# Optimization experiments

Hardware: AMD Instinct MI355X
Metric: run time of the kernel (lower is better)

## Reference

```python
import jax, jax.numpy as jnp
import numpy as np

EPS = 1e-5
K_UP = 5      # k_upsample
SCALE = 2

def _conv(x, w, pad):
    # NCHW conv, no bias
    return jax.lax.conv_general_dilated(
        x, w, window_strides=(1, 1), padding=((pad, pad), (pad, pad)),
        dimension_numbers=('NCHW', 'OIHW', 'NCHW'))

def _bn(x, gamma, beta):
    # train-mode BatchNorm2d forward: batch stats over (N,H,W), biased var
    m = x.mean(axis=(0, 2, 3), keepdims=True)
    v = x.var(axis=(0, 2, 3), keepdims=True)
    xn = (x - m) * jax.lax.rsqrt(v + EPS)
    return xn * gamma[None, :, None, None] + beta[None, :, None, None]

def _pixel_shuffle(x, r):
    b, c, h, w = x.shape
    co = c // (r * r)
    x = x.reshape(b, co, r, r, h, w)
    x = x.transpose(0, 1, 4, 2, 5, 3)  # b, co, h, r, w, r
    return x.reshape(b, co, h * r, w * r)

def setup_inputs() -> dict:
    key = jax.random.key(0)
    ks = jax.random.split(key, 3)
    b, c, h, w = 8, 128, 64, 64
    mid = 64
    return {
        'x': jax.random.normal(ks[0], (b, c, h, w), jnp.float32),
        'comp_w': jax.random.normal(ks[1], (mid, c, 1, 1), jnp.float32) * (1.0 / np.sqrt(c)),
        'comp_g': jnp.ones((mid,), jnp.float32),
        'comp_b': jnp.zeros((mid,), jnp.float32),
        'enc_w': jax.random.normal(ks[2], ((K_UP * SCALE) ** 2, mid, 3, 3), jnp.float32) * (1.0 / np.sqrt(mid * 9)),
        'enc_g': jnp.ones(((K_UP * SCALE) ** 2,), jnp.float32),
        'enc_b': jnp.zeros(((K_UP * SCALE) ** 2,), jnp.float32),
    }

def reference(x, comp_w, comp_g, comp_b, enc_w, enc_g, enc_b):
    b, c, h, w = x.shape
    hm, wm = h * SCALE, w * SCALE
    # --- kernel prediction branch ---
    t = jax.nn.silu(_bn(_conv(x, comp_w, 0), comp_g, comp_b))        # [b,64,h,w]
    t = _bn(_conv(t, enc_w, 1), enc_g, enc_b)                        # [b,100,h,w] (act=False)
    t = _pixel_shuffle(t, SCALE)                                     # [b,25,hm,wm]
    wgt = jax.nn.softmax(t, axis=1)                                  # [b,25,hm,wm]
    # --- feature reassembly branch ---
    x_up = jnp.repeat(jnp.repeat(x, SCALE, axis=2), SCALE, axis=3)   # nearest upsample
    pad = (K_UP // 2) * SCALE  # = 4, preserves hm x wm with dilation=SCALE
    xp = jnp.pad(x_up, ((0, 0), (0, 0), (pad, pad), (pad, pad)))
    # unfold: kernel K_UP, dilation SCALE -> [b, c, 25, hm, wm], taps in (kh, kw) order
    patches = jnp.stack(
        [xp[:, :, dy * SCALE:dy * SCALE + hm, dx * SCALE:dx * SCALE + wm]
         for dy in range(K_UP) for dx in range(K_UP)], axis=2)
    # content-aware weighted sum over the 25 taps
    return jnp.einsum('bkhw,bckhw->bchw', wgt, patches)
```

## Files before the change

kernel.cpp:

```cpp
#include <hip/hip_runtime.h>
#include <hip/hip_bf16.h>
#include <math.h>

#define C_   128
#define HW_  4096
#define OC_  100
#define NSTAT_ 32768.0f

typedef __bf16 bf16x8 __attribute__((ext_vector_type(8)));
typedef __bf16 bf16x4 __attribute__((ext_vector_type(4)));
typedef float  f32x4  __attribute__((ext_vector_type(4)));

__global__ __launch_bounds__(256, 4) void k_conv1(const float* __restrict__ x,
                                                  const float* __restrict__ w,
                                                  const float* __restrict__ wenc,
                                                  __bf16* __restrict__ t1c,
                                                  float* __restrict__ csum,
                                                  float* __restrict__ csq,
                                                  __bf16* __restrict__ wprep) {
    __shared__ __bf16 xt[64 * 128];
    __shared__ __bf16 wt[64 * 128];
    __shared__ float sS[64], sQ[64];

    int blk = blockIdx.x;
    int b = blk & 7;
    int chunk = blk >> 3;
    int px0 = chunk * 64;
    int tid = threadIdx.x;
    if (tid < 64) { sS[tid] = 0.f; sQ[tid] = 0.f; }

    if (blk < 63) {
#pragma unroll
        for (int u = 0; u < 4; ++u) {
            int idx = blk * 1024 + u * 256 + tid;
            int oc = idx / 576, k = idx - oc * 576;
            int tap = k >> 6, ic = k & 63;
            wprep[idx] = (oc < OC_) ? (__bf16)wenc[((size_t)oc * 64 + ic) * 9 + tap]
                                    : (__bf16)0.f;
        }
    }

#pragma unroll
    for (int it = 0; it < 8; ++it) {
        int j = it * 256 + tid;
        int oc = j >> 5, f = j & 31;
        float4 v = *(const float4*)(w + (size_t)oc * 128 + f * 4);
        int blki = (f >> 1) ^ (oc & 15);
        bf16x4 st;
        st[0] = (__bf16)v.x; st[1] = (__bf16)v.y; st[2] = (__bf16)v.z; st[3] = (__bf16)v.w;
        *(bf16x4*)&wt[oc * 128 + blki * 8 + (f & 1) * 4] = st;
    }
#pragma unroll
    for (int it = 0; it < 2; ++it) {
        int j = it * 256 + tid;
        int px4 = (j & 15) * 4, icq = j >> 4;
        const float* xp = x + ((size_t)b * C_ + icq * 4) * HW_ + px0 + px4;
        float4 v0 = *(const float4*)(xp);
        float4 v1 = *(const float4*)(xp + HW_);
        float4 v2 = *(const float4*)(xp + 2 * HW_);
        float4 v3 = *(const float4*)(xp + 3 * HW_);
        float r0[4] = {v0.x, v0.y, v0.z, v0.w};
        float r1[4] = {v1.x, v1.y, v1.z, v1.w};
        float r2_[4] = {v2.x, v2.y, v2.z, v2.w};
        float r3[4] = {v3.x, v3.y, v3.z, v3.w};
#pragma unroll
        for (int r2 = 0; r2 < 4; ++r2) {
            int px = px4 + r2;
            int blki = (icq >> 1) ^ (px & 15);
            bf16x4 st;
            st[0] = (__bf16)r0[r2]; st[1] = (__bf16)r1[r2];
            st[2] = (__bf16)r2_[r2]; st[3] = (__bf16)r3[r2];
            *(bf16x4*)&xt[px * 128 + blki * 8 + (icq & 1) * 4] = st;
        }
    }
    __syncthreads();

    int lane = tid & 63, wv = tid >> 6;
    int p = lane & 15, q = lane >> 4;

    f32x4 acc[4];
#pragma unroll
    for (int n = 0; n < 4; ++n) acc[n] = (f32x4){0.f, 0.f, 0.f, 0.f};

#pragma unroll
    for (int kk = 0; kk < 4; ++kk) {
        int blki = (kk * 4 + q) ^ p;
        bf16x8 a = *(const bf16x8*)&xt[(wv * 16 + p) * 128 + blki * 8];
#pragma unroll
        for (int n = 0; n < 4; ++n) {
            bf16x8 bb = *(const bf16x8*)&wt[(n * 16 + p) * 128 + blki * 8];
            acc[n] = __builtin_amdgcn_mfma_f32_16x16x32_bf16(a, bb, acc[n], 0, 0, 0);
        }
    }

    __bf16* t1b = t1c + ((size_t)b * HW_ + px0 + wv * 16) * 64;
#pragma unroll
    for (int n = 0; n < 4; ++n) {
        float s = 0.f, qq = 0.f;
#pragma unroll
        for (int rg = 0; rg < 4; ++rg) {
            float v = acc[n][rg];
            t1b[(size_t)(q * 4 + rg) * 64 + n * 16 + p] = (__bf16)v;
            s += v; qq += v * v;
        }
        s += __shfl_down(s, 32, 64);  s += __shfl_down(s, 16, 64);
        qq += __shfl_down(qq, 32, 64); qq += __shfl_down(qq, 16, 64);
        if (lane < 16) {
            atomicAdd(&sS[n * 16 + p], s);
            atomicAdd(&sQ[n * 16 + p], qq);
        }
    }
    __syncthreads();
    if (tid < 64) {
        atomicAdd(&csum[tid], sS[tid]);
        atomicAdd(&csq[tid], sQ[tid]);
    }
}

__global__ __launch_bounds__(256, 4) void k_conv3(const __bf16* __restrict__ t1c,
                                                  const __bf16* __restrict__ wprep,
                                                  const float* __restrict__ csum,
                                                  const float* __restrict__ csq,
                                                  const float* __restrict__ cg,
                                                  const float* __restrict__ cb,
                                                  float* __restrict__ t2c,
                                                  float* __restrict__ esum,
                                                  float* __restrict__ esq) {
    __shared__ __bf16 xt[10 * 10 * 72];
    __shared__ __bf16 bt[2][112 * 32];
    __shared__ float lsc[64], lsh[64];
    __shared__ float esuml[112], esql[112];

    int blk = blockIdx.x;
    int b = blk & 7;
    int tile = blk >> 3;
    int ty0 = (tile >> 3) * 8, tx0 = (tile & 7) * 8;
    int tid = threadIdx.x;
    if (tid < 112) { esuml[tid] = 0.f; esql[tid] = 0.f; }
    if (tid >= 128 && tid < 192) {
        int c = tid - 128;
        float invN = 1.0f / NSTAT_;
        float m = csum[c] * invN;
        float v = csq[c] * invN - m * m;
        float rs = rsqrtf(v + 1e-5f);
        float sc = cg[c] * rs;
        lsc[c] = sc;
        lsh[c] = cb[c] - m * sc;
    }
    __syncthreads();

    {
        int oc = tid >> 2, part = tid & 3;
        *(bf16x8*)&bt[0][oc * 32 + part * 8] =
            *(const bf16x8*)(wprep + (size_t)oc * 576 + part * 8);
        if (tid < 192) {
            int c1 = tid + 256;
            int oc1 = c1 >> 2, p1 = c1 & 3;
            *(bf16x8*)&bt[0][oc1 * 32 + p1 * 8] =
                *(const bf16x8*)(wprep + (size_t)oc1 * 576 + p1 * 8);
        }
    }

    const __bf16* tb = t1c + (size_t)b * HW_ * 64;
#pragma unroll
    for (int it = 0; it < 7; ++it) {
        int idx = it * 256 + tid;
        if (idx < 1600) {
            int pxi = idx >> 4, f4 = idx & 15;
            int yy = pxi / 10, xx = pxi - yy * 10;
            int gy = ty0 + yy - 1, gx = tx0 + xx - 1;
            float o0 = 0.f, o1 = 0.f, o2 = 0.f, o3 = 0.f;
            if (gy >= 0 && gy < 64 && gx >= 0 && gx < 64) {
                bf16x4 v = *(const bf16x4*)(tb + ((size_t)(gy << 6) + gx) * 64 + f4 * 4);
                float4 sc = *(const float4*)(lsc + f4 * 4);
                float4 sh = *(const float4*)(lsh + f4 * 4);
                float u;
                u = fmaf((float)v[0], sc.x, sh.x); o0 = u / (1.f + __expf(-u));
                u = fmaf((float)v[1], sc.y, sh.y); o1 = u / (1.f + __expf(-u));
                u = fmaf((float)v[2], sc.z, sh.z); o2 = u / (1.f + __expf(-u));
                u = fmaf((float)v[3], sc.w, sh.w); o3 = u / (1.f + __expf(-u));
            }
            bf16x4 st;
            st[0] = (__bf16)o0; st[1] = (__bf16)o1; st[2] = (__bf16)o2; st[3] = (__bf16)o3;
            *(bf16x4*)&xt[pxi * 72 + f4 * 4] = st;
        }
    }
    __syncthreads();

    int lane = tid & 63, wv = tid >> 6;
    int p = lane & 15, q = lane >> 4;
    int ya = 2 * wv + (p >> 3), xa = p & 7;
    int soc = tid >> 2, spart = tid & 3;
    int soc1 = (tid + 256) >> 2, spart1 = (tid + 256) & 3;

    f32x4 acc[7];
#pragma unroll
    for (int n = 0; n < 7; ++n) acc[n] = (f32x4){0.f, 0.f, 0.f, 0.f};

#pragma unroll
    for (int kk = 0; kk < 18; ++kk) {
        const int cur = kk & 1;
        bf16x8 r0, r1;
        if (kk < 17) {
            r0 = *(const bf16x8*)(wprep + (size_t)soc * 576 + (kk + 1) * 32 + spart * 8);
            if (tid < 192)
                r1 = *(const bf16x8*)(wprep + (size_t)soc1 * 576 + (kk + 1) * 32 + spart1 * 8);
        }
        const int tap = kk >> 1, ich = (kk & 1) * 32;
        const int ky = tap / 3, kx = tap - ky * 3;
        bf16x8 a0 = *(const bf16x8*)&xt[((ya + ky) * 10 + xa + kx) * 72 + ich + q * 8];
#pragma unroll
        for (int n = 0; n < 7; ++n) {
            bf16x8 bb = *(const bf16x8*)&bt[cur][(n * 16 + p) * 32 + q * 8];
            acc[n] = __builtin_amdgcn_mfma_f32_16x16x32_bf16(a0, bb, acc[n], 0, 0, 0);
        }
        if (kk < 17) {
            *(bf16x8*)&bt[1 - cur][soc * 32 + spart * 8] = r0;
            if (tid < 192)
                *(bf16x8*)&bt[1 - cur][soc1 * 32 + spart1 * 8] = r1;
            __syncthreads();
        }
    }

    float* t2b = t2c + (size_t)b * 25 * HW_ * 4;
#pragma unroll
    for (int n = 0; n < 7; ++n) {
        int oc = n * 16 + p;
        int k5 = oc >> 2, sch = oc & 3;
        bool wr = oc < OC_;
        float s = 0.f, qq = 0.f;
#pragma unroll
        for (int rg = 0; rg < 4; ++rg) {
            int mp = q * 4 + rg;
            int y = ty0 + 2 * wv + (mp >> 3), xo = tx0 + (mp & 7);
            float v = acc[n][rg];
            if (wr) t2b[((size_t)k5 * HW_ + (y << 6) + xo) * 4 + sch] = v;
            s += v; qq += v * v;
        }
        s += __shfl_down(s, 32, 64);  s += __shfl_down(s, 16, 64);
        qq += __shfl_down(qq, 32, 64); qq += __shfl_down(qq, 16, 64);
        if (lane < 16) {
            atomicAdd(&esuml[n * 16 + lane], s);
            atomicAdd(&esql[n * 16 + lane], qq);
        }
    }
    __syncthreads();
    if (tid < 112) {
        atomicAdd(&esum[tid], esuml[tid]);
        atomicAdd(&esq[tid], esql[tid]);
    }
}

__global__ __launch_bounds__(512, 2) void k_carafe(const float* __restrict__ x,
                                                   const float* __restrict__ t2c,
                                                   const float* __restrict__ esum,
                                                   const float* __restrict__ esq,
                                                   const float* __restrict__ eg,
                                                   const float* __restrict__ eb,
                                                   float* __restrict__ out) {
    __shared__ float xt[400 * 20];
    __shared__ float esc[112], esh[112];

    int blk = blockIdx.x;
    int b = blk & 7;
    int r = blk >> 3;
    int tile = r & 15;
    int cq = r >> 4;
    int tx0 = (tile & 3) * 16, ty0 = (tile >> 2) * 16;
    int tid = threadIdx.x;
    if (tid < 112) {
        float invN = 1.0f / NSTAT_;
        float m = esum[tid] * invN;
        float v = esq[tid] * invN - m * m;
        float rs = rsqrtf(v + 1e-5f);
        float sc = (tid < OC_) ? eg[tid] * rs : 0.f;
        esc[tid] = sc;
        esh[tid] = (tid < OC_) ? eb[tid] - m * sc : 0.f;
    }

    int t0 = tid & 1, px = tid >> 1;
    int pxx = px & 15, py = px >> 4;
    int iy = ty0 + py, jx = tx0 + pxx;
    int pxl = (iy << 6) + jx;

    const float* xb = x + (size_t)b * C_ * HW_;

    f32x4 pf[4];
#pragma unroll
    for (int it = 0; it < 4; ++it) {
        int idx = it * 512 + tid;
        if (idx < 1600) {
            int c4 = idx / 400;
            int hp = idx - c4 * 400;
            int yy = hp / 20, xx = hp - yy * 20;
            int gy = ty0 - 2 + yy, gx = tx0 - 2 + xx;
            f32x4 st = {0.f, 0.f, 0.f, 0.f};
            if (gy >= 0 && gy < 64 && gx >= 0 && gx < 64) {
                size_t base = (size_t)(cq * 32 + c4 * 4) * HW_ + (gy << 6) + gx;
                st[0] = xb[base];
                st[1] = xb[base + HW_];
                st[2] = xb[base + 2 * HW_];
                st[3] = xb[base + 3 * HW_];
            }
            pf[it] = st;
        }
    }
    __syncthreads();

    float wA[25], wB[25];
    {
        const float* t2p = t2c + (size_t)b * 25 * HW_ * 4 + (size_t)pxl * 4 + 2 * t0;
        int cA = 2 * t0, cB = 2 * t0 + 1;
        float mxA = -1e30f, mxB = -1e30f;
#pragma unroll
        for (int k = 0; k < 25; ++k) {
            float2 v = *(const float2*)(t2p + (size_t)k * HW_ * 4);
            float lA = fmaf(v.x, esc[4 * k + cA], esh[4 * k + cA]);
            float lB = fmaf(v.y, esc[4 * k + cB], esh[4 * k + cB]);
            wA[k] = lA; wB[k] = lB;
            mxA = fmaxf(mxA, lA); mxB = fmaxf(mxB, lB);
        }
        float sA = 0.f, sB = 0.f;
#pragma unroll
        for (int k = 0; k < 25; ++k) {
            float eA = __expf(wA[k] - mxA);
            float eB = __expf(wB[k] - mxB);
            wA[k] = eA; wB[k] = eB;
            sA += eA; sB += eB;
        }
        float iA = 1.f / sA, iB = 1.f / sB;
#pragma unroll
        for (int k = 0; k < 25; ++k) { wA[k] *= iA; wB[k] *= iB; }
    }

#pragma unroll
    for (int it = 0; it < 4; ++it) {
        int idx = it * 512 + tid;
        if (idx < 1600) {
            int c4 = idx / 400;
            int hp = idx - c4 * 400;
            *(f32x4*)&xt[hp * 20 + c4 * 4] = pf[it];
        }
    }
    __syncthreads();

    int i0 = iy * 2 + t0;
    float* op = out + (size_t)b * C_ * 16384 + (size_t)i0 * 128 + jx * 2;
    int cbase = cq * 32;

    f32x4 pg[4];
#pragma unroll
    for (int it = 0; it < 4; ++it) {
        int idx = it * 512 + tid;
        if (idx < 1600) {
            int c4 = idx / 400;
            int hp = idx - c4 * 400;
            int yy = hp / 20, xx = hp - yy * 20;
            int gy = ty0 - 2 + yy, gx = tx0 - 2 + xx;
            f32x4 st = {0.f, 0.f, 0.f, 0.f};
            if (gy >= 0 && gy < 64 && gx >= 0 && gx < 64) {
                size_t base = (size_t)(cbase + 16 + c4 * 4) * HW_ + (gy << 6) + gx;
                st[0] = xb[base];
                st[1] = xb[base + HW_];
                st[2] = xb[base + 2 * HW_];
                st[3] = xb[base + 3 * HW_];
            }
            pg[it] = st;
        }
    }

    {
        float accA[16], accB[16];
#pragma unroll
        for (int e = 0; e < 16; ++e) { accA[e] = 0.f; accB[e] = 0.f; }
#pragma unroll
        for (int dy = 0; dy < 5; ++dy)
#pragma unroll
            for (int dx = 0; dx < 5; ++dx) {
                int pos = (py + dy) * 20 + pxx + dx;
                float a = wA[dy * 5 + dx], bw = wB[dy * 5 + dx];
#pragma unroll
                for (int c4 = 0; c4 < 4; ++c4) {
                    f32x4 xv = *(const f32x4*)&xt[pos * 20 + c4 * 4];
                    accA[c4 * 4 + 0] = fmaf(a, xv[0], accA[c4 * 4 + 0]);
                    accA[c4 * 4 + 1] = fmaf(a, xv[1], accA[c4 * 4 + 1]);
                    accA[c4 * 4 + 2] = fmaf(a, xv[2], accA[c4 * 4 + 2]);
                    accA[c4 * 4 + 3] = fmaf(a, xv[3], accA[c4 * 4 + 3]);
                    accB[c4 * 4 + 0] = fmaf(bw, xv[0], accB[c4 * 4 + 0]);
                    accB[c4 * 4 + 1] = fmaf(bw, xv[1], accB[c4 * 4 + 1]);
                    accB[c4 * 4 + 2] = fmaf(bw, xv[2], accB[c4 * 4 + 2]);
                    accB[c4 * 4 + 3] = fmaf(bw, xv[3], accB[c4 * 4 + 3]);
                }
            }
#pragma unroll
        for (int e = 0; e < 16; ++e) {
            float2 st2;
            st2.x = accA[e]; st2.y = accB[e];
            *(float2*)&op[(size_t)(cbase + e) * 16384] = st2;
        }
    }
    __syncthreads();

#pragma unroll
    for (int it = 0; it < 4; ++it) {
        int idx = it * 512 + tid;
        if (idx < 1600) {
            int c4 = idx / 400;
            int hp = idx - c4 * 400;
            *(f32x4*)&xt[hp * 20 + c4 * 4] = pg[it];
        }
    }
    __syncthreads();

    {
        float accA[16], accB[16];
#pragma unroll
        for (int e = 0; e < 16; ++e) { accA[e] = 0.f; accB[e] = 0.f; }
#pragma unroll
        for (int dy = 0; dy < 5; ++dy)
#pragma unroll
            for (int dx = 0; dx < 5; ++dx) {
                int pos = (py + dy) * 20 + pxx + dx;
                float a = wA[dy * 5 + dx], bw = wB[dy * 5 + dx];
#pragma unroll
                for (int c4 = 0; c4 < 4; ++c4) {
                    f32x4 xv = *(const f32x4*)&xt[pos * 20 + c4 * 4];
                    accA[c4 * 4 + 0] = fmaf(a, xv[0], accA[c4 * 4 + 0]);
                    accA[c4 * 4 + 1] = fmaf(a, xv[1], accA[c4 * 4 + 1]);
                    accA[c4 * 4 + 2] = fmaf(a, xv[2], accA[c4 * 4 + 2]);
                    accA[c4 * 4 + 3] = fmaf(a, xv[3], accA[c4 * 4 + 3]);
                    accB[c4 * 4 + 0] = fmaf(bw, xv[0], accB[c4 * 4 + 0]);
                    accB[c4 * 4 + 1] = fmaf(bw, xv[1], accB[c4 * 4 + 1]);
                    accB[c4 * 4 + 2] = fmaf(bw, xv[2], accB[c4 * 4 + 2]);
                    accB[c4 * 4 + 3] = fmaf(bw, xv[3], accB[c4 * 4 + 3]);
                }
            }
#pragma unroll
        for (int e = 0; e < 16; ++e) {
            float2 st2;
            st2.x = accA[e]; st2.y = accB[e];
            *(float2*)&op[(size_t)(cbase + 16 + e) * 16384] = st2;
        }
    }
}

extern "C" void kernel_launch(void* const* d_in, const int* in_sizes, int n_in,
                              void* d_out, int out_size, void* d_ws, size_t ws_size,
                              hipStream_t stream) {
    const float* x      = (const float*)d_in[0];
    const float* comp_w = (const float*)d_in[1];
    const float* comp_g = (const float*)d_in[2];
    const float* comp_b = (const float*)d_in[3];
    const float* enc_w  = (const float*)d_in[4];
    const float* enc_g  = (const float*)d_in[5];
    const float* enc_b  = (const float*)d_in[6];
    float* out = (float*)d_out;

    float* ws = (float*)d_ws;
    __bf16* t1c = (__bf16*)ws;
    float* t2c  = ws + 1048576;
    float* st   = ws + 1048576 + 3670016;
    float* csum = st;
    float* csq  = st + 64;
    float* esum = st + 128;
    float* esq  = st + 240;
    __bf16* wprep = (__bf16*)(st + 352);

    hipMemsetAsync(st, 0, 352 * sizeof(float), stream);
    k_conv1<<<512, 256, 0, stream>>>(x, comp_w, enc_w, t1c, csum, csq, wprep);
    k_conv3<<<512, 256, 0, stream>>>(t1c, wprep, csum, csq, comp_g, comp_b, t2c, esum, esq);
    k_carafe<<<512, 512, 0, stream>>>(x, t2c, esum, esq, enc_g, enc_b, out);
}
```

Measured before the change: 158.7 us.

## Read conv3 weights directly from global and stage output tile through LDS

The k_conv3 kernel no longer double-buffers the encoder weights in shared memory with a barrier per K-step. Each lane now loads its MFMA B-fragment straight from global memory (relying on cache). The accumulator results are written into the reused input-tile LDS buffer and then stored to global as coalesced 16-byte vectors instead of scattered scalar stores. This removes 17 barriers and the LDS weight footprint, at the cost of more global/L2 weight traffic per wave.

```diff
diff --git a/kernel.cpp b/kernel.cpp
--- a/kernel.cpp
+++ b/kernel.cpp
@@ -126,8 +126,8 @@
                                                   float* __restrict__ t2c,
                                                   float* __restrict__ esum,
                                                   float* __restrict__ esq) {
-    __shared__ __bf16 xt[10 * 10 * 72];
-    __shared__ __bf16 bt[2][112 * 32];
+    __shared__ float xtf[25 * 260];
+    __bf16* xt = (__bf16*)xtf;
     __shared__ float lsc[64], lsh[64];
     __shared__ float esuml[112], esql[112];
 
@@ -148,18 +148,6 @@
         lsh[c] = cb[c] - m * sc;
     }
     __syncthreads();
-
-    {
-        int oc = tid >> 2, part = tid & 3;
-        *(bf16x8*)&bt[0][oc * 32 + part * 8] =
-            *(const bf16x8*)(wprep + (size_t)oc * 576 + part * 8);
-        if (tid < 192) {
-            int c1 = tid + 256;
-            int oc1 = c1 >> 2, p1 = c1 & 3;
-            *(bf16x8*)&bt[0][oc1 * 32 + p1 * 8] =
-                *(const bf16x8*)(wprep + (size_t)oc1 * 576 + p1 * 8);
-        }
-    }
 
     const __bf16* tb = t1c + (size_t)b * HW_ * 64;
 #pragma unroll
@@ -190,8 +178,7 @@
     int lane = tid & 63, wv = tid >> 6;
     int p = lane & 15, q = lane >> 4;
     int ya = 2 * wv + (p >> 3), xa = p & 7;
-    int soc = tid >> 2, spart = tid & 3;
-    int soc1 = (tid + 256) >> 2, spart1 = (tid + 256) & 3;
+    const __bf16* wpl = wprep + p * 576 + q * 8;
 
     f32x4 acc[7];
 #pragma unroll
@@ -199,30 +186,17 @@
 
 #pragma unroll
     for (int kk = 0; kk < 18; ++kk) {
-        const int cur = kk & 1;
-        bf16x8 r0, r1;
-        if (kk < 17) {
-            r0 = *(const bf16x8*)(wprep + (size_t)soc * 576 + (kk + 1) * 32 + spart * 8);
-            if (tid < 192)
-                r1 = *(const bf16x8*)(wprep + (size_t)soc1 * 576 + (kk + 1) * 32 + spart1 * 8);
-        }
         const int tap = kk >> 1, ich = (kk & 1) * 32;
         const int ky = tap / 3, kx = tap - ky * 3;
         bf16x8 a0 = *(const bf16x8*)&xt[((ya + ky) * 10 + xa + kx) * 72 + ich + q * 8];
 #pragma unroll
         for (int n = 0; n < 7; ++n) {
-            bf16x8 bb = *(const bf16x8*)&bt[cur][(n * 16 + p) * 32 + q * 8];
+            bf16x8 bb = *(const bf16x8*)(wpl + n * 9216 + kk * 32);
             acc[n] = __builtin_amdgcn_mfma_f32_16x16x32_bf16(a0, bb, acc[n], 0, 0, 0);
         }
-        if (kk < 17) {
-            *(bf16x8*)&bt[1 - cur][soc * 32 + spart * 8] = r0;
-            if (tid < 192)
-                *(bf16x8*)&bt[1 - cur][soc1 * 32 + spart1 * 8] = r1;
-            __syncthreads();
-        }
-    }
-
-    float* t2b = t2c + (size_t)b * 25 * HW_ * 4;
+    }
+    __syncthreads();
+
 #pragma unroll
     for (int n = 0; n < 7; ++n) {
         int oc = n * 16 + p;
@@ -232,9 +206,8 @@
 #pragma unroll
         for (int rg = 0; rg < 4; ++rg) {
             int mp = q * 4 + rg;
-            int y = ty0 + 2 * wv + (mp >> 3), xo = tx0 + (mp & 7);
             float v = acc[n][rg];
-            if (wr) t2b[((size_t)k5 * HW_ + (y << 6) + xo) * 4 + sch] = v;
+            if (wr) xtf[k5 * 260 + (2 * wv + (mp >> 3)) * 32 + (mp & 7) * 4 + sch] = v;
             s += v; qq += v * v;
         }
         s += __shfl_down(s, 32, 64);  s += __shfl_down(s, 16, 64);
@@ -245,6 +218,18 @@
         }
     }
     __syncthreads();
+
+    float* t2b = t2c + (size_t)b * 25 * HW_ * 4;
+#pragma unroll
+    for (int it = 0; it < 7; ++it) {
+        int idx = it * 256 + tid;
+        if (idx < 1600) {
+            int k5 = idx >> 6, pix = idx & 63;
+            f32x4 v = *(const f32x4*)&xtf[k5 * 260 + pix * 4];
+            int gy = ty0 + (pix >> 3), gx = tx0 + (pix & 7);
+            *(f32x4*)&t2b[((size_t)k5 * HW_ + (gy << 6) + gx) * 4] = v;
+        }
+    }
     if (tid < 112) {
         atomicAdd(&esum[tid], esuml[tid]);
         atomicAdd(&esq[tid], esql[tid]);
```

Result: slower. 177.3 us (+11.7%).
